# Optimization experiments

Measured on AMD Instinct MI355X. Metric: run time of the kernel, lower is better.

The kernel has to match this reference:

```python
import jax, jax.numpy as jnp
import numpy as np

B, N, M = 4, 50000, 256
BIN_MIN, BIN_MAX = -3.0, 3.0


def setup_inputs() -> dict:
    key = jax.random.key(0)
    kx, ky = jax.random.split(key)
    x_coords = jax.random.normal(kx, (B, N), dtype=jnp.float32)
    y_coords = jax.random.normal(ky, (B, N), dtype=jnp.float32)
    bins = jnp.linspace(BIN_MIN, BIN_MAX, M, dtype=jnp.float32)
    return {"x_coords": x_coords, "y_coords": y_coords, "bins": bins}


def reference(x_coords, y_coords, bins):
    # bandwidth defaults to bin resolution (bins[1] - bins[0])
    bandwidth = bins[1] - bins[0]
    # per-axis Gaussian kernel values: (B, N, M)
    kx = jnp.exp(-0.5 * jnp.square((x_coords[..., None] - bins) / bandwidth))
    ky = jnp.exp(-0.5 * jnp.square((y_coords[..., None] - bins) / bandwidth))
    # joint kernel values reduced over particles: (B, M, M)
    joint = jnp.einsum("bni,bnj->bij", kx, ky)
    norm = jnp.sum(joint, axis=(-2, -1), keepdims=True) + 1e-10
    return joint / norm
```

## Files before the change

### kernel.cpp

```cpp
#include <hip/hip_runtime.h>


#define B_     4
#define N_     50000
#define M_     256
#define BK     64
#define NCH    48
#define KSTEPS 17
#define KCH    (KSTEPS * BK)
#define LDKB   80
#define ROWS   129
#define AXB    (ROWS * LDKB)
#define BUFB   (2 * AXB)
#define BLOCK  256
#define WINB   7
#define CS2    0.72134752f
#define HINV   0.36787944f

#if __has_builtin(__builtin_amdgcn_exp2f)
  #define EXP2(t) __builtin_amdgcn_exp2f(t)
#else
  #define EXP2(t) exp2f(t)
#endif

typedef __attribute__((ext_vector_type(4))) int i32x4;

__device__ __forceinline__ unsigned short bf16ru(float f) {
    return (unsigned short)((__builtin_bit_cast(unsigned, f) + 0x8000u) >> 16);
}
__device__ __forceinline__ float bf2f(unsigned short u) {
    return __builtin_bit_cast(float, ((unsigned)u) << 16);
}

template<int MT, int R0, bool SCAT>
__device__ __forceinline__ float chunk_loop(
    char* __restrict__ tb, const float* __restrict__ coord,
    int k0, int rowlo, int colbase, float bin0, float invbw,
    int ilo, int jlo, int wj, int lm, int quad, int tid,
    unsigned short* __restrict__ pb)
{
    i32x4 acc[MT][4];
    #pragma unroll
    for (int mt = 0; mt < MT; ++mt)
        #pragma unroll
        for (int nt = 0; nt < 4; ++nt) acc[mt][nt] = i32x4{0, 0, 0, 0};

    int ps0 = 1 << 20, ps1 = 1 << 20;

    float v0 = 3.0e30f, vnext = 3.0e30f;
    if (SCAT) {
        const int kcol = tid & 63;
        const int ka = k0 + kcol;       if (ka  < N_) v0    = coord[ka];
        const int kb2 = k0 + BK + kcol; if (kb2 < N_) vnext = coord[kb2];
    }
    __syncthreads();

    if (SCAT) {
        const float u  = (v0 - bin0) * invbw;
        const float st = rintf(u) - 3.0f;
        const float d0 = u - st;
        float E = 127.0f * EXP2(-CS2 * d0 * d0);
        float G = EXP2(fmaf(d0 + d0, CS2, -CS2));
        int rr = (int)st - rowlo;
        ps0 = rr;
        const int dmp = colbase + 128 * LDKB;
        #pragma unroll
        for (int j = 0; j < WINB; ++j) {
            tb[((unsigned)rr < 128u) ? (colbase + rr * LDKB) : dmp] =
                (char)(int)(E + 0.5f);
            E *= G; G *= HINV; ++rr;
        }
    }
    __syncthreads();

    for (int ks = 0; ks < KSTEPS; ++ks) {
        const int q = ks & 1;
        float vpre = 3.0e30f;
        if (SCAT && (ks + 2) < KSTEPS) {
            const int ka = k0 + (ks + 2) * BK + (tid & 63);
            if (ka < N_) vpre = coord[ka];
        }
        if (SCAT && (ks + 1) < KSTEPS) {
            const int qn  = q ^ 1;
            const int bqn = qn * BUFB + colbase;
            const int dmp = bqn + 128 * LDKB;
            const int ps  = qn ? ps1 : ps0;
            if (ps < (1 << 19)) {
                #pragma unroll
                for (int j = 0; j < WINB; ++j) {
                    const int rr = ps + j;
                    tb[((unsigned)rr < 128u) ? (bqn + rr * LDKB) : dmp] = 0;
                }
            }
            const float u  = (vnext - bin0) * invbw;
            const float st = rintf(u) - 3.0f;
            const float d0 = u - st;
            float E = 127.0f * EXP2(-CS2 * d0 * d0);
            float G = EXP2(fmaf(d0 + d0, CS2, -CS2));
            int rr = (int)st - rowlo;
            if (qn) ps1 = rr; else ps0 = rr;
            #pragma unroll
            for (int j = 0; j < WINB; ++j) {
                tb[((unsigned)rr < 128u) ? (bqn + rr * LDKB) : dmp] =
                    (char)(int)(E + 0.5f);
                E *= G; G *= HINV; ++rr;
            }
        }
        vnext = vpre;

        const char* bufA = tb + q * BUFB;
        const char* bufB = tb + q * BUFB + AXB;
        i32x4 af[MT], bfr[4];
        #pragma unroll
        for (int t4 = 0; t4 < MT; ++t4)
            af[t4] = *(const i32x4*)(bufA + (R0 + t4 * 16 + lm) * LDKB + quad * 16);
        #pragma unroll
        for (int t4 = 0; t4 < 4; ++t4)
            bfr[t4] = *(const i32x4*)(bufB + (wj + t4 * 16 + lm) * LDKB + quad * 16);
        #pragma unroll
        for (int mt = 0; mt < MT; ++mt)
            #pragma unroll
            for (int nt = 0; nt < 4; ++nt)
                acc[mt][nt] = __builtin_amdgcn_mfma_i32_16x16x64_i8(
                    af[mt], bfr[nt], acc[mt][nt], 0, 0, 0);
        __syncthreads();
    }

    float tsum = 0.f;
    #pragma unroll
    for (int mt = 0; mt < MT; ++mt) {
        const int row0 = ilo + R0 + mt * 16 + quad * 4;
        #pragma unroll
        for (int nt = 0; nt < 4; ++nt) {
            const int col = jlo + wj + nt * 16 + lm;
            const i32x4 a = acc[mt][nt];
            #pragma unroll
            for (int e = 0; e < 4; ++e) {
                const float v = (float)a[e];
                pb[(size_t)(row0 + e) * M_ + col] = bf16ru(v);
                tsum += v;
            }
        }
    }
    return tsum;
}

__global__ __launch_bounds__(BLOCK) void kde_gemm(
    const float* __restrict__ xs, const float* __restrict__ ys,
    const float* __restrict__ bins, unsigned short* __restrict__ partial,
    float* __restrict__ ws2, int wide)
{
    __shared__ __align__(16) char tiles[2][2][ROWS][LDKB];
    __shared__ float sred[4];

    const int tid   = threadIdx.x;
    const int tile  = blockIdx.x;
    const int chunk = blockIdx.y;
    const int b     = blockIdx.z;

    const int ilo = (tile & 1) * 128;
    const int jlo = (tile >> 1) * 128;
    const float bin0  = bins[0];
    const float invbw = 1.0f / (bins[1] - bin0);

    {
        int4* za = (int4*)&tiles[0][0][0][0];
        const int4 z4 = {0, 0, 0, 0};
        for (int t = tid; t < (int)(sizeof(tiles) / 16); t += BLOCK) za[t] = z4;
    }

    const int  axis    = (tid >> 6) & 1;
    const int  rowlo   = axis ? jlo : ilo;
    const int  colbase = axis * AXB + (tid & 63);
    const float* coord = (axis ? ys : xs) + b * N_;
    const int  k0 = chunk * KCH;
    char* const tb = &tiles[0][0][0][0];

    const int w    = tid >> 6;
    const int wj   = (w & 1) * 64;
    const int lane = tid & 63;
    const int lm   = lane & 15;
    const int quad = lane >> 4;
    unsigned short* pb = partial + (((size_t)chunk * B_ + b) << 16);

    float tsum;
    if (w < 2)
        tsum = chunk_loop<3, 0, true >(tb, coord, k0, rowlo, colbase, bin0, invbw,
                                       ilo, jlo, wj, lm, quad, tid, pb);
    else
        tsum = chunk_loop<5, 48, false>(tb, coord, k0, rowlo, colbase, bin0, invbw,
                                       ilo, jlo, wj, lm, quad, tid, pb);

    #pragma unroll
    for (int off = 32; off; off >>= 1) tsum += __shfl_xor(tsum, off);
    if (lane == 0) sred[w] = tsum;
    __syncthreads();
    if (tid == 0) {
        const float bsum = sred[0] + sred[1] + sred[2] + sred[3];
        if (wide) {
            const int bid = (b * NCH + chunk) * 4 + tile;
            ws2[bid] = bsum;
        } else {
            atomicAdd(&ws2[b], bsum);
        }
    }
}

__global__ __launch_bounds__(BLOCK) void kde_tail(
    const unsigned short* __restrict__ partial, const float* __restrict__ ws2,
    float* __restrict__ out, int wide)
{
    __shared__ float sred[4];
    __shared__ float snorm;
    const int tid = threadIdx.x;
    const int cellIdx = blockIdx.x * BLOCK + tid;
    const int bb = cellIdx >> 14;
    const int cb = cellIdx & 16383;

    float nrm;
    if (wide) {
        float t = (tid < 4 * NCH) ? ws2[bb * 4 * NCH + tid] : 0.f;
        #pragma unroll
        for (int off = 32; off; off >>= 1) t += __shfl_xor(t, off);
        if ((tid & 63) == 0) sred[tid >> 6] = t;
        __syncthreads();
        if (tid == 0) snorm = sred[0] + sred[1] + sred[2] + sred[3];
        __syncthreads();
        nrm = snorm;
    } else {
        nrm = ws2[bb];
    }

    float4 a = {0.f, 0.f, 0.f, 0.f};
    #pragma unroll 4
    for (int c = 0; c < NCH; ++c) {
        const ushort4 v = *(const ushort4*)(partial +
            (((size_t)c * B_ + bb) << 16) + (size_t)cb * 4);
        a.x += bf2f(v.x); a.y += bf2f(v.y); a.z += bf2f(v.z); a.w += bf2f(v.w);
    }
    const float sc = 1.0f / (nrm + 1e-10f);
    a.x *= sc; a.y *= sc; a.z *= sc; a.w *= sc;
    ((float4*)out)[cellIdx] = a;
}

extern "C" void kernel_launch(void* const* d_in, const int* in_sizes, int n_in,
                              void* d_out, int out_size, void* d_ws, size_t ws_size,
                              hipStream_t stream)
{
    const float* xs   = (const float*)d_in[0];
    const float* ys   = (const float*)d_in[1];
    const float* bins = (const float*)d_in[2];
    float* out = (float*)d_out;
    unsigned short* partial = (unsigned short*)d_ws;
    const size_t PSZ = (size_t)NCH * B_ * M_ * M_ * sizeof(unsigned short);
    float* ws2 = (float*)((char*)d_ws + PSZ);

    const int wide = (ws_size >= PSZ + 4096) ? 1 : 0;
    if (!wide) hipMemsetAsync(ws2, 0, 4 * sizeof(float), stream);

    kde_gemm<<<dim3(4, NCH, B_), dim3(BLOCK), 0, stream>>>(
        xs, ys, bins, partial, ws2, wide);
    kde_tail<<<dim3(B_ * M_ * M_ / (4 * BLOCK)), dim3(BLOCK), 0, stream>>>(
        partial, ws2, out, wide);
}
```

Measured before the change: 90.29 us.

## Spread kernel-window scatter across all four waves with balanced MFMA tiles

Before, waves 0-1 did all of the Gaussian window scatter into LDS while waves 2-3 carried a larger share of the MFMA work (5 row tiles against 3). Now every thread handles the scatter: each pair of threads splits the 7-entry window (4 and 3 entries), and each value is computed directly as exp2 of a quadratic plus a log2(127) offset instead of by a multiplicative recurrence. All waves then do an equal 4x4 MFMA tile. This aims to balance work across waves and shorten the serial scatter path, at the cost of more exp2 calls and more threads issuing byte stores to LDS.

```diff
diff --git a/kernel.cpp b/kernel.cpp
--- a/kernel.cpp
+++ b/kernel.cpp
@@ -15,7 +15,7 @@
 #define BLOCK  256
 #define WINB   7
 #define CS2    0.72134752f
-#define HINV   0.36787944f
+#define L127   6.9886847f
 
 #if __has_builtin(__builtin_amdgcn_exp2f)
   #define EXP2(t) __builtin_amdgcn_exp2f(t)
@@ -32,43 +32,81 @@
     return __builtin_bit_cast(float, ((unsigned)u) << 16);
 }
 
-template<int MT, int R0, bool SCAT>
-__device__ __forceinline__ float chunk_loop(
-    char* __restrict__ tb, const float* __restrict__ coord,
-    int k0, int rowlo, int colbase, float bin0, float invbw,
-    int ilo, int jlo, int wj, int lm, int quad, int tid,
-    unsigned short* __restrict__ pb)
+__global__ __launch_bounds__(BLOCK) void kde_gemm(
+    const float* __restrict__ xs, const float* __restrict__ ys,
+    const float* __restrict__ bins, unsigned short* __restrict__ partial,
+    float* __restrict__ ws2, int wide)
 {
-    i32x4 acc[MT][4];
+    __shared__ __align__(16) char tiles[2][2][ROWS][LDKB];
+    __shared__ float sred[4];
+
+    const int tid   = threadIdx.x;
+    const int tile  = blockIdx.x;
+    const int chunk = blockIdx.y;
+    const int b     = blockIdx.z;
+
+    const int ilo = (tile & 1) * 128;
+    const int jlo = (tile >> 1) * 128;
+    const float bin0  = bins[0];
+    const float invbw = 1.0f / (bins[1] - bin0);
+
+    {
+        int4* za = (int4*)&tiles[0][0][0][0];
+        const int4 z4 = {0, 0, 0, 0};
+        for (int t = tid; t < (int)(sizeof(tiles) / 16); t += BLOCK) za[t] = z4;
+    }
+
+    const int  h       = tid & 1;
+    const int  jn      = 4 - h;
+    const int  jbase   = h << 2;
+    const int  kcol    = (tid >> 1) & 63;
+    const int  axis    = (tid >> 7) & 1;
+    const int  rowlo   = axis ? jlo : ilo;
+    const int  colbase = axis * AXB + kcol;
+    const float* coord = (axis ? ys : xs) + b * N_;
+    const int  k0 = chunk * KCH;
+    char* const tb = &tiles[0][0][0][0];
+
+    const int w    = tid >> 6;
+    const int R0   = (w >> 1) * 64;
+    const int wj   = (w & 1) * 64;
+    const int lane = tid & 63;
+    const int lm   = lane & 15;
+    const int quad = lane >> 4;
+    unsigned short* pb = partial + (((size_t)chunk * B_ + b) << 16);
+
+    i32x4 acc[4][4];
     #pragma unroll
-    for (int mt = 0; mt < MT; ++mt)
+    for (int mt = 0; mt < 4; ++mt)
         #pragma unroll
         for (int nt = 0; nt < 4; ++nt) acc[mt][nt] = i32x4{0, 0, 0, 0};
 
     int ps0 = 1 << 20, ps1 = 1 << 20;
 
     float v0 = 3.0e30f, vnext = 3.0e30f;
-    if (SCAT) {
-        const int kcol = tid & 63;
+    {
         const int ka = k0 + kcol;       if (ka  < N_) v0    = coord[ka];
         const int kb2 = k0 + BK + kcol; if (kb2 < N_) vnext = coord[kb2];
     }
     __syncthreads();
 
-    if (SCAT) {
+    {
         const float u  = (v0 - bin0) * invbw;
         const float st = rintf(u) - 3.0f;
         const float d0 = u - st;
-        float E = 127.0f * EXP2(-CS2 * d0 * d0);
-        float G = EXP2(fmaf(d0 + d0, CS2, -CS2));
-        int rr = (int)st - rowlo;
-        ps0 = rr;
+        const int rr0 = (int)st - rowlo;
+        ps0 = rr0;
         const int dmp = colbase + 128 * LDKB;
         #pragma unroll
-        for (int j = 0; j < WINB; ++j) {
-            tb[((unsigned)rr < 128u) ? (colbase + rr * LDKB) : dmp] =
-                (char)(int)(E + 0.5f);
-            E *= G; G *= HINV; ++rr;
+        for (int j = 0; j < 4; ++j) {
+            if (j < jn) {
+                const int jj = jbase + j;
+                const float d = d0 - (float)jj;
+                const float E = EXP2(fmaf(-CS2 * d, d, L127));
+                const int rr = rr0 + jj;
+                tb[((unsigned)rr < 128u) ? (colbase + rr * LDKB) : dmp] =
+                    (char)(int)(E + 0.5f);
+            }
         }
     }
     __syncthreads();
@@ -76,49 +114,54 @@
     for (int ks = 0; ks < KSTEPS; ++ks) {
         const int q = ks & 1;
         float vpre = 3.0e30f;
-        if (SCAT && (ks + 2) < KSTEPS) {
-            const int ka = k0 + (ks + 2) * BK + (tid & 63);
+        if ((ks + 2) < KSTEPS) {
+            const int ka = k0 + (ks + 2) * BK + kcol;
             if (ka < N_) vpre = coord[ka];
         }
-        if (SCAT && (ks + 1) < KSTEPS) {
+        if ((ks + 1) < KSTEPS) {
             const int qn  = q ^ 1;
             const int bqn = qn * BUFB + colbase;
             const int dmp = bqn + 128 * LDKB;
             const int ps  = qn ? ps1 : ps0;
             if (ps < (1 << 19)) {
                 #pragma unroll
-                for (int j = 0; j < WINB; ++j) {
-                    const int rr = ps + j;
-                    tb[((unsigned)rr < 128u) ? (bqn + rr * LDKB) : dmp] = 0;
+                for (int j = 0; j < 4; ++j) {
+                    if (j < jn) {
+                        const int rr = ps + jbase + j;
+                        tb[((unsigned)rr < 128u) ? (bqn + rr * LDKB) : dmp] = 0;
+                    }
                 }
             }
             const float u  = (vnext - bin0) * invbw;
             const float st = rintf(u) - 3.0f;
             const float d0 = u - st;
-            float E = 127.0f * EXP2(-CS2 * d0 * d0);
-            float G = EXP2(fmaf(d0 + d0, CS2, -CS2));
-            int rr = (int)st - rowlo;
-            if (qn) ps1 = rr; else ps0 = rr;
+            const int rr0 = (int)st - rowlo;
+            if (qn) ps1 = rr0; else ps0 = rr0;
             #pragma unroll
-            for (int j = 0; j < WINB; ++j) {
-                tb[((unsigned)rr < 128u) ? (bqn + rr * LDKB) : dmp] =
-                    (char)(int)(E + 0.5f);
-                E *= G; G *= HINV; ++rr;
+            for (int j = 0; j < 4; ++j) {
+                if (j < jn) {
+                    const int jj = jbase + j;
+                    const float d = d0 - (float)jj;
+                    const float E = EXP2(fmaf(-CS2 * d, d, L127));
+                    const int rr = rr0 + jj;
+                    tb[((unsigned)rr < 128u) ? (bqn + rr * LDKB) : dmp] =
+                        (char)(int)(E + 0.5f);
+                }
             }
         }
         vnext = vpre;
 
         const char* bufA = tb + q * BUFB;
         const char* bufB = tb + q * BUFB + AXB;
-        i32x4 af[MT], bfr[4];
-        #pragma unroll
-        for (int t4 = 0; t4 < MT; ++t4)
+        i32x4 af[4], bfr[4];
+        #pragma unroll
+        for (int t4 = 0; t4 < 4; ++t4)
             af[t4] = *(const i32x4*)(bufA + (R0 + t4 * 16 + lm) * LDKB + quad * 16);
         #pragma unroll
         for (int t4 = 0; t4 < 4; ++t4)
             bfr[t4] = *(const i32x4*)(bufB + (wj + t4 * 16 + lm) * LDKB + quad * 16);
         #pragma unroll
-        for (int mt = 0; mt < MT; ++mt)
+        for (int mt = 0; mt < 4; ++mt)
             #pragma unroll
             for (int nt = 0; nt < 4; ++nt)
                 acc[mt][nt] = __builtin_amdgcn_mfma_i32_16x16x64_i8(
@@ -128,7 +171,7 @@
 
     float tsum = 0.f;
     #pragma unroll
-    for (int mt = 0; mt < MT; ++mt) {
+    for (int mt = 0; mt < 4; ++mt) {
         const int row0 = ilo + R0 + mt * 16 + quad * 4;
         #pragma unroll
         for (int nt = 0; nt < 4; ++nt) {
@@ -142,54 +185,6 @@
             }
         }
     }
-    return tsum;
-}
-
-__global__ __launch_bounds__(BLOCK) void kde_gemm(
-    const float* __restrict__ xs, const float* __restrict__ ys,
-    const float* __restrict__ bins, unsigned short* __restrict__ partial,
-    float* __restrict__ ws2, int wide)
-{
-    __shared__ __align__(16) char tiles[2][2][ROWS][LDKB];
-    __shared__ float sred[4];
-
-    const int tid   = threadIdx.x;
-    const int tile  = blockIdx.x;
-    const int chunk = blockIdx.y;
-    const int b     = blockIdx.z;
-
-    const int ilo = (tile & 1) * 128;
-    const int jlo = (tile >> 1) * 128;
-    const float bin0  = bins[0];
-    const float invbw = 1.0f / (bins[1] - bin0);
-
-    {
-        int4* za = (int4*)&tiles[0][0][0][0];
-        const int4 z4 = {0, 0, 0, 0};
-        for (int t = tid; t < (int)(sizeof(tiles) / 16); t += BLOCK) za[t] = z4;
-    }
-
-    const int  axis    = (tid >> 6) & 1;
-    const int  rowlo   = axis ? jlo : ilo;
-    const int  colbase = axis * AXB + (tid & 63);
-    const float* coord = (axis ? ys : xs) + b * N_;
-    const int  k0 = chunk * KCH;
-    char* const tb = &tiles[0][0][0][0];
-
-    const int w    = tid >> 6;
-    const int wj   = (w & 1) * 64;
-    const int lane = tid & 63;
-    const int lm   = lane & 15;
-    const int quad = lane >> 4;
-    unsigned short* pb = partial + (((size_t)chunk * B_ + b) << 16);
-
-    float tsum;
-    if (w < 2)
-        tsum = chunk_loop<3, 0, true >(tb, coord, k0, rowlo, colbase, bin0, invbw,
-                                       ilo, jlo, wj, lm, quad, tid, pb);
-    else
-        tsum = chunk_loop<5, 48, false>(tb, coord, k0, rowlo, colbase, bin0, invbw,
-                                       ilo, jlo, wj, lm, quad, tid, pb);
 
     #pragma unroll
     for (int off = 32; off; off >>= 1) tsum += __shfl_xor(tsum, off);
```

Measured after the change: 88.16 us. -2.4%, faster.
